# Kernel tuning notes

Hardware: AMD Instinct MI355X
Metric: run time of the kernel (lower is better)

## Reference

```python
import jax, jax.numpy as jnp
import numpy as np

N = 50000       # nodes
E = 1600000     # edges (before self-loops)
IN = 128        # in_channels
HID = 64        # hidden_channels
HEADS = 2
OUT = 16        # out_channels
NEG_SLOPE = 0.2 # PyG GATConv default leaky_relu slope


def setup_inputs() -> dict:
    key = jax.random.key(0)
    ks = jax.random.split(key, 12)
    g = lambda k, shp, s=0.1: (jax.random.normal(k, shp, dtype=jnp.float32) * s)
    return {
        "x": jax.random.normal(ks[0], (N, IN), dtype=jnp.float32),
        "edge_index": jax.random.randint(ks[1], (2, E), 0, N, dtype=jnp.int32),
        # layer 0: in -> hidden, heads concat
        "W0": g(ks[2], (IN, HEADS * HID)),
        "as0": g(ks[3], (HEADS, HID)),
        "ad0": g(ks[4], (HEADS, HID)),
        "b0": jnp.zeros((HEADS * HID,), jnp.float32),
        # layer 1: hidden*heads -> hidden, heads concat
        "W1": g(ks[5], (HEADS * HID, HEADS * HID)),
        "as1": g(ks[6], (HEADS, HID)),
        "ad1": g(ks[7], (HEADS, HID)),
        "b1": jnp.zeros((HEADS * HID,), jnp.float32),
        # layer 2: hidden*heads -> out, heads averaged (concat=False)
        "W2": g(ks[8], (HEADS * HID, HEADS * OUT)),
        "as2": g(ks[9], (HEADS, OUT)),
        "ad2": g(ks[10], (HEADS, OUT)),
        "b2": jnp.zeros((OUT,), jnp.float32),
    }


def gat_conv(x, src, dst, W, a_src, a_dst, b, concat):
    """PyG-style GATConv (inference; self-loops already in src/dst)."""
    n = x.shape[0]
    H, C = a_src.shape
    h = (x @ W).reshape(n, H, C)                      # [N,H,C]
    alpha_s = jnp.einsum('nhc,hc->nh', h, a_src)      # [N,H]
    alpha_d = jnp.einsum('nhc,hc->nh', h, a_dst)      # [N,H]
    e = alpha_s[src] + alpha_d[dst]                   # [E,H]
    e = jax.nn.leaky_relu(e, NEG_SLOPE)
    # softmax over incoming edges per destination node
    m = jax.ops.segment_max(e, dst, num_segments=n)   # [N,H]
    w = jnp.exp(e - m[dst])                           # [E,H]
    denom = jax.ops.segment_sum(w, dst, num_segments=n)
    alpha = w / (denom[dst] + 1e-16)                  # [E,H]
    out = jax.ops.segment_sum(alpha[:, :, None] * h[src], dst, num_segments=n)  # [N,H,C]
    out = out.reshape(n, H * C) if concat else out.mean(axis=1)
    return out + b


def reference(x, edge_index, W0, as0, ad0, b0, W1, as1, ad1, b1, W2, as2, ad2, b2):
    loop = jnp.arange(N, dtype=edge_index.dtype)
    src = jnp.concatenate([edge_index[0], loop])
    dst = jnp.concatenate([edge_index[1], loop])
    h = jax.nn.elu(gat_conv(x, src, dst, W0, as0, ad0, b0, concat=True))
    h = jax.nn.elu(gat_conv(h, src, dst, W1, as1, ad1, b1, concat=True))
    return gat_conv(h, src, dst, W2, as2, ad2, b2, concat=False)
```

## Files before the change

kernel.cpp:

```cpp
#include <hip/hip_runtime.h>
#include <hip/hip_fp16.h>
#include <cstdint>
#include <cstddef>
#include <type_traits>

constexpr int kN   = 50000;
constexpr int kE   = 1600000;
constexpr int kET  = kE + kN;
constexpr float kNEG = 0.2f;
constexpr int NBUCK = (kN + 127) / 128;
constexpr int CAPB  = 5120;
constexpr int PCHUNK = 2048;
constexpr int PGRID = (kET + PCHUNK - 1) / PCHUNK;

typedef _Float16 f16x8 __attribute__((ext_vector_type(8)));
typedef float    f32x4 __attribute__((ext_vector_type(4)));

__global__ __launch_bounds__(256) void partition_kernel(const int* __restrict__ ei,
                                                        int* __restrict__ bcnt,
                                                        unsigned* __restrict__ part) {
  __shared__ int hist[NBUCK];
  __shared__ int resv[NBUCK];
  __shared__ int lcnt[NBUCK];
  const int t = threadIdx.x;
  for (int i = t; i < NBUCK; i += 256) hist[i] = 0;
  __syncthreads();
  const int c0 = blockIdx.x * PCHUNK;
  const int cend = (c0 + PCHUNK < kET) ? c0 + PCHUNK : kET;
  for (int i = c0 + t; i < cend; i += 256) {
    const int dst = (i < kE) ? ei[kE + i] : (i - kE);
    atomicAdd(&hist[dst >> 7], 1);
  }
  __syncthreads();
  for (int i = t; i < NBUCK; i += 256) {
    lcnt[i] = 0;
    if (hist[i]) resv[i] = i * CAPB + atomicAdd(&bcnt[i], hist[i]);
  }
  __syncthreads();
  for (int i = c0 + t; i < cend; i += 256) {
    int src, dst;
    if (i < kE) { src = ei[i]; dst = ei[kE + i]; }
    else        { src = i - kE; dst = src; }
    const int b = dst >> 7;
    const int off = atomicAdd(&lcnt[b], 1);
    part[resv[b] + off] = ((unsigned)(dst & 127) << 16) | (unsigned)src;
  }
}

__global__ __launch_bounds__(512) void finalize_kernel(const unsigned* __restrict__ part,
                                                       const int* __restrict__ bcnt,
                                                       int* __restrict__ row_beg,
                                                       int* __restrict__ row_cnt,
                                                       int* __restrict__ col_src) {
  __shared__ int cnt[128];
  __shared__ int sc[128];
  __shared__ int nbase[128];
  const int b = blockIdx.x, t = threadIdx.x;
  const int lo = b * CAPB;
  const int hi = lo + bcnt[b];
  if (t < 128) cnt[t] = 0;
  __syncthreads();
  for (int j = lo + t; j < hi; j += 512) atomicAdd(&cnt[part[j] >> 16], 1);
  __syncthreads();
  if (t < 128) sc[t] = cnt[t];
  __syncthreads();
  for (int off = 1; off < 128; off <<= 1) {
    int v = 0;
    if (t < 128 && t >= off) v = sc[t - off];
    __syncthreads();
    if (t < 128) sc[t] += v;
    __syncthreads();
  }
  if (t < 128) {
    const int c = cnt[t];
    nbase[t] = lo + sc[t] - c;
    const int node = b * 128 + t;
    if (node < kN) { row_beg[node] = nbase[t]; row_cnt[node] = c; }
    cnt[t] = 0;
  }
  __syncthreads();
  for (int j = lo + t; j < hi; j += 512) {
    const unsigned v = part[j];
    const int nl = v >> 16;
    const int pos = nbase[nl] + atomicAdd(&cnt[nl], 1);
    col_src[pos] = (int)(v & 0xffffu);
  }
}

__global__ __launch_bounds__(256) void prep_w_kernel(
    const float* __restrict__ W0, const float* __restrict__ W1,
    const float* __restrict__ W2, __half* __restrict__ Wt0,
    __half* __restrict__ Wt1, __half* __restrict__ Wt2) {
  int i = blockIdx.x * 256 + threadIdx.x;
  const int stride = gridDim.x * 256;
  for (; i < 16384 * 2 + 4096; i += stride) {
    if (i < 16384) {
      const int k = i >> 7, c = i & 127;
      Wt0[c * 128 + k] = __float2half_rn(W0[i]);
    } else if (i < 32768) {
      const int j = i - 16384, k = j >> 7, c = j & 127;
      Wt1[c * 128 + k] = __float2half_rn(W1[j]);
    } else {
      const int j = i - 32768, k = j >> 5, c = j & 31;
      Wt2[c * 128 + k] = __float2half_rn(W2[j]);
    }
  }
}

template<int NCOL, typename TIN>
__global__ __launch_bounds__(256) void mfma_transform_kernel(
    const TIN* __restrict__ X, const __half* __restrict__ Wt,
    const float* __restrict__ asf, const float* __restrict__ adf,
    __half* __restrict__ H2, float2* __restrict__ AS, float2* __restrict__ AD, int n) {
  constexpr int NT = NCOL / 16;
  const int wid  = threadIdx.x >> 6;
  const int lane = threadIdx.x & 63;
  const int rbase = blockIdx.x * 64 + wid * 16;
  if (rbase >= n) return;
  const int r  = rbase + (lane & 15);
  const int kg = (lane >> 4) * 8;
  const _Float16* __restrict__ Wf = (const _Float16*)Wt;

  f32x4 acc[NT];
#pragma unroll
  for (int t = 0; t < NT; t++) acc[t] = (f32x4){0.f, 0.f, 0.f, 0.f};

#pragma unroll
  for (int kc = 0; kc < 4; kc++) {
    const int kh = kc * 32 + kg;
    f16x8 bfrag;
    if constexpr (std::is_same<TIN, float>::value) {
      const float4 v0 = *(const float4*)(X + (size_t)r * 128 + kh);
      const float4 v1 = *(const float4*)(X + (size_t)r * 128 + kh + 4);
      bfrag[0] = (_Float16)v0.x; bfrag[1] = (_Float16)v0.y;
      bfrag[2] = (_Float16)v0.z; bfrag[3] = (_Float16)v0.w;
      bfrag[4] = (_Float16)v1.x; bfrag[5] = (_Float16)v1.y;
      bfrag[6] = (_Float16)v1.z; bfrag[7] = (_Float16)v1.w;
    } else {
      bfrag = *(const f16x8*)((const _Float16*)X + (size_t)r * 128 + kh);
    }
#pragma unroll
    for (int t = 0; t < NT; t++) {
      const f16x8 afrag = *(const f16x8*)(Wf + (size_t)(t * 16 + (lane & 15)) * 128 + kh);
      acc[t] = __builtin_amdgcn_mfma_f32_16x16x32_f16(afrag, bfrag, acc[t], 0, 0, 0);
    }
  }

  const int c4 = (lane >> 4) * 4;
  float s0 = 0.f, s1 = 0.f, d0 = 0.f, d1 = 0.f;
#pragma unroll
  for (int t = 0; t < NT; t++) {
    const int c0 = t * 16 + c4;
    const float4 av = *(const float4*)(asf + c0);
    const float4 dv = *(const float4*)(adf + c0);
    const float ps = acc[t][0] * av.x + acc[t][1] * av.y + acc[t][2] * av.z + acc[t][3] * av.w;
    const float pd = acc[t][0] * dv.x + acc[t][1] * dv.y + acc[t][2] * dv.z + acc[t][3] * dv.w;
    if (t < NT / 2) { s0 += ps; d0 += pd; } else { s1 += ps; d1 += pd; }
    union { __half2 h[2]; uint2 u; } pk;
    pk.h[0] = __floats2half2_rn(acc[t][0], acc[t][1]);
    pk.h[1] = __floats2half2_rn(acc[t][2], acc[t][3]);
    *(uint2*)(H2 + (size_t)r * NCOL + c0) = pk.u;
  }
#pragma unroll
  for (int off = 16; off <= 32; off <<= 1) {
    s0 += __shfl_xor(s0, off); s1 += __shfl_xor(s1, off);
    d0 += __shfl_xor(d0, off); d1 += __shfl_xor(d1, off);
  }
  if (lane < 16) {
    AS[rbase + lane] = make_float2(s0, s1);
    AD[rbase + lane] = make_float2(d0, d1);
  }
}

template<int C, int MODE, typename TOUT>
__global__ __launch_bounds__(256) void agg_kernel(
    const __half* __restrict__ H2, const float2* __restrict__ AS,
    const float2* __restrict__ AD, const int* __restrict__ row_beg,
    const int* __restrict__ row_cnt, const int* __restrict__ col_src,
    const float* __restrict__ bias, TOUT* __restrict__ OUT) {
  const int wid  = threadIdx.x >> 6;
  const int lane = threadIdx.x & 63;
  const int node = blockIdx.x * 4 + wid;

  const int begin = row_beg[node];
  const int d = row_cnt[node];
  const float2 adn = AD[node];

  int srcv = 0;
  unsigned pkw = 0;
  float sum0 = 0.f, sum1 = 0.f;
  if (lane < d) {
    srcv = col_src[begin + lane];
    const float2 a = AS[srcv];
    float e0 = a.x + adn.x; e0 = (e0 > 0.f) ? e0 : kNEG * e0;
    float e1 = a.y + adn.y; e1 = (e1 > 0.f) ? e1 : kNEG * e1;
    sum0 = __expf(e0); sum1 = __expf(e1);
    const __half2 ph = __floats2half2_rn(sum0, sum1);
    pkw = *(const unsigned*)&ph;
  }
  for (int j = 64 + lane; j < d; j += 64) {
    const int s = col_src[begin + j];
    const float2 a = AS[s];
    float e0 = a.x + adn.x; e0 = (e0 > 0.f) ? e0 : kNEG * e0;
    float e1 = a.y + adn.y; e1 = (e1 > 0.f) ? e1 : kNEG * e1;
    sum0 += __expf(e0); sum1 += __expf(e1);
  }
#pragma unroll
  for (int off = 32; off >= 1; off >>= 1) {
    sum0 += __shfl_xor(sum0, off);
    sum1 += __shfl_xor(sum1, off);
  }
  const float inv0 = 1.0f / (sum0 + 1e-16f);
  const float inv1 = 1.0f / (sum1 + 1e-16f);

  const int dr = (d < 64) ? d : 64;

  if constexpr (MODE == 0) {
    const int e = lane >> 4;
    const int q = lane & 15;
    const int hsel = (q >= 8);
    const unsigned sel = hsel ? 0x03020302u : 0x01000100u;
    const float inv = hsel ? inv1 : inv0;
    float4 a0 = make_float4(0.f, 0.f, 0.f, 0.f);
    float4 a1 = make_float4(0.f, 0.f, 0.f, 0.f);
    for (int j = 0; j < dr; j += 16) {
      const int j0 = j + e, j1 = j + 4 + e, j2 = j + 8 + e, j3 = j + 12 + e;
      const int s0 = __shfl(srcv, j0), s1 = __shfl(srcv, j1),
                s2 = __shfl(srcv, j2), s3 = __shfl(srcv, j3);
      const unsigned p0 = __shfl((int)pkw, j0), p1 = __shfl((int)pkw, j1),
                     p2 = __shfl((int)pkw, j2), p3 = __shfl((int)pkw, j3);
      union { uint4 u; __half2 h[4]; } r0, r1, r2, r3;
      r0.u = *(const uint4*)(H2 + (size_t)s0 * 128 + 8 * q);
      r1.u = *(const uint4*)(H2 + (size_t)s1 * 128 + 8 * q);
      r2.u = *(const uint4*)(H2 + (size_t)s2 * 128 + 8 * q);
      r3.u = *(const uint4*)(H2 + (size_t)s3 * 128 + 8 * q);
      union { unsigned u; __half2 h; } w0, w1, w2, w3;
      w0.u = __builtin_amdgcn_perm(p0, p0, sel);
      w1.u = __builtin_amdgcn_perm(p1, p1, sel);
      w2.u = __builtin_amdgcn_perm(p2, p2, sel);
      w3.u = __builtin_amdgcn_perm(p3, p3, sel);
      __half2 hz; *(unsigned*)&hz = 0u;
      __half2 hc0 = hz, hc1 = hz, hc2 = hz, hc3 = hz;
      hc0 = __hfma2(w0.h, r0.h[0], hc0); hc1 = __hfma2(w0.h, r0.h[1], hc1);
      hc2 = __hfma2(w0.h, r0.h[2], hc2); hc3 = __hfma2(w0.h, r0.h[3], hc3);
      hc0 = __hfma2(w1.h, r1.h[0], hc0); hc1 = __hfma2(w1.h, r1.h[1], hc1);
      hc2 = __hfma2(w1.h, r1.h[2], hc2); hc3 = __hfma2(w1.h, r1.h[3], hc3);
      hc0 = __hfma2(w2.h, r2.h[0], hc0); hc1 = __hfma2(w2.h, r2.h[1], hc1);
      hc2 = __hfma2(w2.h, r2.h[2], hc2); hc3 = __hfma2(w2.h, r2.h[3], hc3);
      hc0 = __hfma2(w3.h, r3.h[0], hc0); hc1 = __hfma2(w3.h, r3.h[1], hc1);
      hc2 = __hfma2(w3.h, r3.h[2], hc2); hc3 = __hfma2(w3.h, r3.h[3], hc3);
      float2 f;
      f = __half22float2(hc0); a0.x += f.x; a0.y += f.y;
      f = __half22float2(hc1); a0.z += f.x; a0.w += f.y;
      f = __half22float2(hc2); a1.x += f.x; a1.y += f.y;
      f = __half22float2(hc3); a1.z += f.x; a1.w += f.y;
    }
    for (int jt = 64 + e; jt < d; jt += 4) {
      const int s = col_src[begin + jt];
      const float2 a = AS[s];
      float e0 = a.x + adn.x; e0 = (e0 > 0.f) ? e0 : kNEG * e0;
      float e1 = a.y + adn.y; e1 = (e1 > 0.f) ? e1 : kNEG * e1;
      const float w = hsel ? __expf(e1) : __expf(e0);
      union { uint4 u; __half2 h[4]; } raw;
      raw.u = *(const uint4*)(H2 + (size_t)s * 128 + 8 * q);
      const float2 f0 = __half22float2(raw.h[0]);
      const float2 f1 = __half22float2(raw.h[1]);
      const float2 f2 = __half22float2(raw.h[2]);
      const float2 f3 = __half22float2(raw.h[3]);
      a0.x = fmaf(w, f0.x, a0.x); a0.y = fmaf(w, f0.y, a0.y);
      a0.z = fmaf(w, f1.x, a0.z); a0.w = fmaf(w, f1.y, a0.w);
      a1.x = fmaf(w, f2.x, a1.x); a1.y = fmaf(w, f2.y, a1.y);
      a1.z = fmaf(w, f3.x, a1.z); a1.w = fmaf(w, f3.y, a1.w);
    }
#pragma unroll
    for (int off = 32; off >= 16; off >>= 1) {
      a0.x += __shfl_xor(a0.x, off); a0.y += __shfl_xor(a0.y, off);
      a0.z += __shfl_xor(a0.z, off); a0.w += __shfl_xor(a0.w, off);
      a1.x += __shfl_xor(a1.x, off); a1.y += __shfl_xor(a1.y, off);
      a1.z += __shfl_xor(a1.z, off); a1.w += __shfl_xor(a1.w, off);
    }
    if (lane < 16) {
      const int ch = 8 * q;
      const float4 b0v = *(const float4*)(bias + ch);
      const float4 b1v = *(const float4*)(bias + ch + 4);
      float4 o0, o1;
      o0.x = a0.x * inv + b0v.x; o0.y = a0.y * inv + b0v.y;
      o0.z = a0.z * inv + b0v.z; o0.w = a0.w * inv + b0v.w;
      o1.x = a1.x * inv + b1v.x; o1.y = a1.y * inv + b1v.y;
      o1.z = a1.z * inv + b1v.z; o1.w = a1.w * inv + b1v.w;
      o0.x = (o0.x > 0.f) ? o0.x : expm1f(o0.x);
      o0.y = (o0.y > 0.f) ? o0.y : expm1f(o0.y);
      o0.z = (o0.z > 0.f) ? o0.z : expm1f(o0.z);
      o0.w = (o0.w > 0.f) ? o0.w : expm1f(o0.w);
      o1.x = (o1.x > 0.f) ? o1.x : expm1f(o1.x);
      o1.y = (o1.y > 0.f) ? o1.y : expm1f(o1.y);
      o1.z = (o1.z > 0.f) ? o1.z : expm1f(o1.z);
      o1.w = (o1.w > 0.f) ? o1.w : expm1f(o1.w);
      union { __half2 h[4]; uint4 u; } pk;
      pk.h[0] = __floats2half2_rn(o0.x, o0.y);
      pk.h[1] = __floats2half2_rn(o0.z, o0.w);
      pk.h[2] = __floats2half2_rn(o1.x, o1.y);
      pk.h[3] = __floats2half2_rn(o1.z, o1.w);
      *(uint4*)((__half*)OUT + (size_t)node * 128 + ch) = pk.u;
    }
  } else {
    const int e = lane >> 3;
    const int q = lane & 7;
    const int hsel = (q >= 4);
    const unsigned sel = hsel ? 0x03020302u : 0x01000100u;
    const float inv = hsel ? inv1 : inv0;
    __half2 hz; *(unsigned*)&hz = 0u;
    __half2 hc0 = hz, hc1 = hz;
    for (int j = 0; j < dr; j += 16) {
      const int j0 = j + e, j1 = j + 8 + e;
      const int s0 = __shfl(srcv, j0), s1 = __shfl(srcv, j1);
      const unsigned p0 = __shfl((int)pkw, j0), p1 = __shfl((int)pkw, j1);
      union { unsigned u; __half2 h; } w0, w1;
      w0.u = __builtin_amdgcn_perm(p0, p0, sel);
      w1.u = __builtin_amdgcn_perm(p1, p1, sel);
      union { uint2 u; __half2 h[2]; } r0, r1;
      r0.u = *(const uint2*)(H2 + (size_t)s0 * 32 + 4 * q);
      r1.u = *(const uint2*)(H2 + (size_t)s1 * 32 + 4 * q);
      hc0 = __hfma2(w0.h, r0.h[0], hc0); hc1 = __hfma2(w0.h, r0.h[1], hc1);
      hc0 = __hfma2(w1.h, r1.h[0], hc0); hc1 = __hfma2(w1.h, r1.h[1], hc1);
    }
    float4 acc;
    float2 f;
    f = __half22float2(hc0); acc.x = f.x; acc.y = f.y;
    f = __half22float2(hc1); acc.z = f.x; acc.w = f.y;
    for (int jt = 64 + e; jt < d; jt += 8) {
      const int s = col_src[begin + jt];
      const float2 a = AS[s];
      float e0 = a.x + adn.x; e0 = (e0 > 0.f) ? e0 : kNEG * e0;
      float e1 = a.y + adn.y; e1 = (e1 > 0.f) ? e1 : kNEG * e1;
      const float w = hsel ? __expf(e1) : __expf(e0);
      union { uint2 u; __half2 h[2]; } raw;
      raw.u = *(const uint2*)(H2 + (size_t)s * 32 + 4 * q);
      const float2 f0 = __half22float2(raw.h[0]);
      const float2 f1 = __half22float2(raw.h[1]);
      acc.x = fmaf(w, f0.x, acc.x); acc.y = fmaf(w, f0.y, acc.y);
      acc.z = fmaf(w, f1.x, acc.z); acc.w = fmaf(w, f1.y, acc.w);
    }
#pragma unroll
    for (int off = 32; off >= 8; off >>= 1) {
      acc.x += __shfl_xor(acc.x, off); acc.y += __shfl_xor(acc.y, off);
      acc.z += __shfl_xor(acc.z, off); acc.w += __shfl_xor(acc.w, off);
    }
    acc.x *= inv; acc.y *= inv; acc.z *= inv; acc.w *= inv;
    const float px = __shfl_xor(acc.x, 4);
    const float py = __shfl_xor(acc.y, 4);
    const float pz = __shfl_xor(acc.z, 4);
    const float pw2 = __shfl_xor(acc.w, 4);
    if (lane < 4) {
      const int ch = 4 * q;
      const float4 bv = *(const float4*)(bias + ch);
      float4 o;
      o.x = 0.5f * (acc.x + px) + bv.x;
      o.y = 0.5f * (acc.y + py) + bv.y;
      o.z = 0.5f * (acc.z + pz) + bv.z;
      o.w = 0.5f * (acc.w + pw2) + bv.w;
      *(float4*)((float*)OUT + (size_t)node * 16 + ch) = o;
    }
  }
}

extern "C" void kernel_launch(void* const* d_in, const int* in_sizes, int n_in,
                              void* d_out, int out_size, void* d_ws, size_t ws_size,
                              hipStream_t stream) {
  const float* x   = (const float*)d_in[0];
  const int*   ei  = (const int*)d_in[1];
  const float* W0  = (const float*)d_in[2];
  const float* as0 = (const float*)d_in[3];
  const float* ad0 = (const float*)d_in[4];
  const float* b0  = (const float*)d_in[5];
  const float* W1  = (const float*)d_in[6];
  const float* as1 = (const float*)d_in[7];
  const float* ad1 = (const float*)d_in[8];
  const float* b1  = (const float*)d_in[9];
  const float* W2  = (const float*)d_in[10];
  const float* as2 = (const float*)d_in[11];
  const float* ad2 = (const float*)d_in[12];
  const float* b2  = (const float*)d_in[13];
  float* out = (float*)d_out;

  size_t off = 0;
  auto alloc = [&](size_t bytes) -> void* {
    void* p = (char*)d_ws + off;
    off += (bytes + 255) & ~(size_t)255;
    return p;
  };
  int*    row_beg = (int*)alloc(sizeof(int) * kN);
  int*    row_cnt = (int*)alloc(sizeof(int) * kN);
  int*    bcnt    = (int*)alloc(sizeof(int) * NBUCK);
  int*    col_src = (int*)alloc(sizeof(int) * (size_t)NBUCK * CAPB);
  float2* AS      = (float2*)alloc(sizeof(float2) * kN);
  float2* AD      = (float2*)alloc(sizeof(float2) * kN);
  __half* H2      = (__half*)alloc(sizeof(__half) * (size_t)kN * 128);
  __half* actA    = (__half*)alloc(sizeof(__half) * (size_t)kN * 128);
  __half* actB    = (__half*)alloc(sizeof(__half) * (size_t)kN * 128);
  __half* Wt0     = (__half*)alloc(sizeof(__half) * 128 * 128);
  __half* Wt1     = (__half*)alloc(sizeof(__half) * 128 * 128);
  __half* Wt2     = (__half*)alloc(sizeof(__half) * 32 * 128);
  unsigned* part  = (unsigned*)actA;
  (void)ws_size; (void)in_sizes; (void)n_in; (void)out_size;

  hipMemsetAsync(bcnt, 0, sizeof(int) * NBUCK, stream);
  prep_w_kernel<<<144, 256, 0, stream>>>(W0, W1, W2, Wt0, Wt1, Wt2);
  partition_kernel<<<PGRID, 256, 0, stream>>>(ei, bcnt, part);
  finalize_kernel<<<NBUCK, 512, 0, stream>>>(part, bcnt, row_beg, row_cnt, col_src);

  const int tgrid = (kN + 63) / 64;
  const int ngrid = kN / 4;

  mfma_transform_kernel<128, float><<<tgrid, 256, 0, stream>>>(x, Wt0, as0, ad0, H2, AS, AD, kN);
  agg_kernel<64, 0, __half><<<ngrid, 256, 0, stream>>>(H2, AS, AD, row_beg, row_cnt, col_src, b0, actA);

  mfma_transform_kernel<128, __half><<<tgrid, 256, 0, stream>>>(actA, Wt1, as1, ad1, H2, AS, AD, kN);
  agg_kernel<64, 0, __half><<<ngrid, 256, 0, stream>>>(H2, AS, AD, row_beg, row_cnt, col_src, b1, actB);

  mfma_transform_kernel<32, __half><<<tgrid, 256, 0, stream>>>(actB, Wt2, as2, ad2, H2, AS, AD, kN);
  agg_kernel<16, 1, float><<<ngrid, 256, 0, stream>>>(H2, AS, AD, row_beg, row_cnt, col_src, b2, out);
}
```

Before: 252.3 us.

## Split hidden features into column quarters and precompute packed normalized edge weights

For the two 128-wide layers, the transform kernel now writes features as four column-quarter slabs, each N×32 halves. A new weight kernel computes the softmax-normalized attention weights per head and packs each one with its 16-bit source index into a record array. A new aggregation kernel then processes one quarter per block, with block ordering chosen so concurrent blocks gather from a single slab. The aim is better cache locality for the gathers and less exponent work inside the aggregation. In exchange it adds an extra kernel launch, writes and reads two record arrays per layer, accumulates fully in fp16, and relies on node ids fitting in 16 bits.

```diff
diff --git a/kernel.cpp b/kernel.cpp
--- a/kernel.cpp
+++ b/kernel.cpp
@@ -12,6 +12,7 @@
 constexpr int CAPB  = 5120;
 constexpr int PCHUNK = 2048;
 constexpr int PGRID = (kET + PCHUNK - 1) / PCHUNK;
+constexpr int QSTRIDE = kN * 32;
 
 typedef _Float16 f16x8 __attribute__((ext_vector_type(8)));
 typedef float    f32x4 __attribute__((ext_vector_type(4)));
@@ -159,7 +160,13 @@
     union { __half2 h[2]; uint2 u; } pk;
     pk.h[0] = __floats2half2_rn(acc[t][0], acc[t][1]);
     pk.h[1] = __floats2half2_rn(acc[t][2], acc[t][3]);
-    *(uint2*)(H2 + (size_t)r * NCOL + c0) = pk.u;
+    if constexpr (NCOL == 128) {
+      const int qq = c0 >> 5;
+      const int co = c0 & 31;
+      *(uint2*)(H2 + (size_t)qq * QSTRIDE + (size_t)r * 32 + co) = pk.u;
+    } else {
+      *(uint2*)(H2 + (size_t)r * NCOL + c0) = pk.u;
+    }
   }
 #pragma unroll
   for (int off = 16; off <= 32; off <<= 1) {
@@ -172,16 +179,162 @@
   }
 }
 
-template<int C, int MODE, typename TOUT>
-__global__ __launch_bounds__(256) void agg_kernel(
+__global__ __launch_bounds__(256) void weight_kernel(
+    const float2* __restrict__ AS, const float2* __restrict__ AD,
+    const int* __restrict__ row_beg, const int* __restrict__ row_cnt,
+    const int* __restrict__ col_src,
+    unsigned* __restrict__ rec0, unsigned* __restrict__ rec1) {
+  const int wid  = threadIdx.x >> 6;
+  const int lane = threadIdx.x & 63;
+  const int node = blockIdx.x * 4 + wid;
+  const int begin = row_beg[node];
+  const int d = row_cnt[node];
+  const float2 adn = AD[node];
+
+  int srcv = 0;
+  float w0 = 0.f, w1 = 0.f;
+  if (lane < d) {
+    srcv = col_src[begin + lane];
+    const float2 a = AS[srcv];
+    float e0 = a.x + adn.x; e0 = (e0 > 0.f) ? e0 : kNEG * e0;
+    float e1 = a.y + adn.y; e1 = (e1 > 0.f) ? e1 : kNEG * e1;
+    w0 = __expf(e0); w1 = __expf(e1);
+  }
+  float sum0 = w0, sum1 = w1;
+  for (int j = 64 + lane; j < d; j += 64) {
+    const int s = col_src[begin + j];
+    const float2 a = AS[s];
+    float e0 = a.x + adn.x; e0 = (e0 > 0.f) ? e0 : kNEG * e0;
+    float e1 = a.y + adn.y; e1 = (e1 > 0.f) ? e1 : kNEG * e1;
+    sum0 += __expf(e0); sum1 += __expf(e1);
+  }
+#pragma unroll
+  for (int off = 32; off >= 1; off >>= 1) {
+    sum0 += __shfl_xor(sum0, off);
+    sum1 += __shfl_xor(sum1, off);
+  }
+  const float inv0 = 1.0f / (sum0 + 1e-16f);
+  const float inv1 = 1.0f / (sum1 + 1e-16f);
+  if (lane < d) {
+    const unsigned h0 = (unsigned)__half_as_ushort(__float2half_rn(w0 * inv0));
+    const unsigned h1 = (unsigned)__half_as_ushort(__float2half_rn(w1 * inv1));
+    rec0[begin + lane] = (unsigned)srcv | (h0 << 16);
+    rec1[begin + lane] = (unsigned)srcv | (h1 << 16);
+  }
+  for (int j = 64 + lane; j < d; j += 64) {
+    const int s = col_src[begin + j];
+    const float2 a = AS[s];
+    float e0 = a.x + adn.x; e0 = (e0 > 0.f) ? e0 : kNEG * e0;
+    float e1 = a.y + adn.y; e1 = (e1 > 0.f) ? e1 : kNEG * e1;
+    const unsigned h0 = (unsigned)__half_as_ushort(__float2half_rn(__expf(e0) * inv0));
+    const unsigned h1 = (unsigned)__half_as_ushort(__float2half_rn(__expf(e1) * inv1));
+    rec0[begin + j] = (unsigned)s | (h0 << 16);
+    rec1[begin + j] = (unsigned)s | (h1 << 16);
+  }
+}
+
+__global__ __launch_bounds__(256) void agg64q_kernel(
+    const __half* __restrict__ H2q, const unsigned* __restrict__ rec0,
+    const unsigned* __restrict__ rec1, const int* __restrict__ row_beg,
+    const int* __restrict__ row_cnt, const float* __restrict__ bias,
+    __half* __restrict__ OUT) {
+  const int bid = blockIdx.x;
+  const int qtr = (bid & 7) >> 1;
+  const int ng  = ((bid >> 3) << 1) | (bid & 1);
+  const int wid  = threadIdx.x >> 6;
+  const int lane = threadIdx.x & 63;
+  const int node = ng * 4 + wid;
+  const int begin = row_beg[node];
+  const int d = row_cnt[node];
+  const unsigned* __restrict__ rec = (qtr >= 2) ? rec1 : rec0;
+  const __half* __restrict__ Hq = H2q + (size_t)qtr * QSTRIDE;
+  const int strm = lane >> 2;
+  const int cq   = lane & 3;
+
+  const unsigned recreg = (lane < d) ? rec[begin + lane] : 0u;
+
+  __half2 hz; *(unsigned*)&hz = 0u;
+  __half2 hc0 = hz, hc1 = hz, hc2 = hz, hc3 = hz;
+  {
+    const unsigned r0 = (unsigned)__shfl((int)recreg, strm);
+    const unsigned r1 = (unsigned)__shfl((int)recreg, 16 + strm);
+    const unsigned r2 = (unsigned)__shfl((int)recreg, 32 + strm);
+    const unsigned r3 = (unsigned)__shfl((int)recreg, 48 + strm);
+    union { uint4 u; __half2 h[4]; } v0, v1, v2, v3;
+    v0.u = *(const uint4*)(Hq + (size_t)(r0 & 0xffffu) * 32 + (cq << 3));
+    v1.u = *(const uint4*)(Hq + (size_t)(r1 & 0xffffu) * 32 + (cq << 3));
+    v2.u = *(const uint4*)(Hq + (size_t)(r2 & 0xffffu) * 32 + (cq << 3));
+    v3.u = *(const uint4*)(Hq + (size_t)(r3 & 0xffffu) * 32 + (cq << 3));
+    union { unsigned u; __half2 h; } w0, w1, w2, w3;
+    w0.u = __builtin_amdgcn_perm(r0, r0, 0x03020302u);
+    w1.u = __builtin_amdgcn_perm(r1, r1, 0x03020302u);
+    w2.u = __builtin_amdgcn_perm(r2, r2, 0x03020302u);
+    w3.u = __builtin_amdgcn_perm(r3, r3, 0x03020302u);
+    hc0 = __hfma2(w0.h, v0.h[0], hc0); hc1 = __hfma2(w0.h, v0.h[1], hc1);
+    hc2 = __hfma2(w0.h, v0.h[2], hc2); hc3 = __hfma2(w0.h, v0.h[3], hc3);
+    hc0 = __hfma2(w1.h, v1.h[0], hc0); hc1 = __hfma2(w1.h, v1.h[1], hc1);
+    hc2 = __hfma2(w1.h, v1.h[2], hc2); hc3 = __hfma2(w1.h, v1.h[3], hc3);
+    hc0 = __hfma2(w2.h, v2.h[0], hc0); hc1 = __hfma2(w2.h, v2.h[1], hc1);
+    hc2 = __hfma2(w2.h, v2.h[2], hc2); hc3 = __hfma2(w2.h, v2.h[3], hc3);
+    hc0 = __hfma2(w3.h, v3.h[0], hc0); hc1 = __hfma2(w3.h, v3.h[1], hc1);
+    hc2 = __hfma2(w3.h, v3.h[2], hc2); hc3 = __hfma2(w3.h, v3.h[3], hc3);
+  }
+  for (int jt = 64 + strm; jt < d; jt += 16) {
+    const unsigned r = rec[begin + jt];
+    union { unsigned u; __half2 h; } wv;
+    wv.u = __builtin_amdgcn_perm(r, r, 0x03020302u);
+    union { uint4 u; __half2 h[4]; } raw;
+    raw.u = *(const uint4*)(Hq + (size_t)(r & 0xffffu) * 32 + (cq << 3));
+    hc0 = __hfma2(wv.h, raw.h[0], hc0);
+    hc1 = __hfma2(wv.h, raw.h[1], hc1);
+    hc2 = __hfma2(wv.h, raw.h[2], hc2);
+    hc3 = __hfma2(wv.h, raw.h[3], hc3);
+  }
+#pragma unroll
+  for (int off = 4; off <= 32; off <<= 1) {
+    union { __half2 h; int i; } a0, a1, a2, a3;
+    a0.h = hc0; a1.h = hc1; a2.h = hc2; a3.h = hc3;
+    a0.i = __shfl_xor(a0.i, off); a1.i = __shfl_xor(a1.i, off);
+    a2.i = __shfl_xor(a2.i, off); a3.i = __shfl_xor(a3.i, off);
+    hc0 = __hadd2(hc0, a0.h); hc1 = __hadd2(hc1, a1.h);
+    hc2 = __hadd2(hc2, a2.h); hc3 = __hadd2(hc3, a3.h);
+  }
+  if (lane < 4) {
+    const int ch = qtr * 32 + lane * 8;
+    const float4 b0v = *(const float4*)(bias + ch);
+    const float4 b1v = *(const float4*)(bias + ch + 4);
+    const float2 f0 = __half22float2(hc0);
+    const float2 f1 = __half22float2(hc1);
+    const float2 f2 = __half22float2(hc2);
+    const float2 f3 = __half22float2(hc3);
+    float4 o0, o1;
+    o0.x = f0.x + b0v.x; o0.y = f0.y + b0v.y; o0.z = f1.x + b0v.z; o0.w = f1.y + b0v.w;
+    o1.x = f2.x + b1v.x; o1.y = f2.y + b1v.y; o1.z = f3.x + b1v.z; o1.w = f3.y + b1v.w;
+    o0.x = (o0.x > 0.f) ? o0.x : expm1f(o0.x);
+    o0.y = (o0.y > 0.f) ? o0.y : expm1f(o0.y);
+    o0.z = (o0.z > 0.f) ? o0.z : expm1f(o0.z);
+    o0.w = (o0.w > 0.f) ? o0.w : expm1f(o0.w);
+    o1.x = (o1.x > 0.f) ? o1.x : expm1f(o1.x);
+    o1.y = (o1.y > 0.f) ? o1.y : expm1f(o1.y);
+    o1.z = (o1.z > 0.f) ? o1.z : expm1f(o1.z);
+    o1.w = (o1.w > 0.f) ? o1.w : expm1f(o1.w);
+    union { __half2 h[4]; uint4 u; } pk;
+    pk.h[0] = __floats2half2_rn(o0.x, o0.y);
+    pk.h[1] = __floats2half2_rn(o0.z, o0.w);
+    pk.h[2] = __floats2half2_rn(o1.x, o1.y);
+    pk.h[3] = __floats2half2_rn(o1.z, o1.w);
+    *(uint4*)(OUT + (size_t)node * 128 + ch) = pk.u;
+  }
+}
+
+__global__ __launch_bounds__(256) void agg16_kernel(
     const __half* __restrict__ H2, const float2* __restrict__ AS,
     const float2* __restrict__ AD, const int* __restrict__ row_beg,
     const int* __restrict__ row_cnt, const int* __restrict__ col_src,
-    const float* __restrict__ bias, TOUT* __restrict__ OUT) {
+    const float* __restrict__ bias, float* __restrict__ OUT) {
   const int wid  = threadIdx.x >> 6;
   const int lane = threadIdx.x & 63;
   const int node = blockIdx.x * 4 + wid;
-
   const int begin = row_beg[node];
   const int d = row_cnt[node];
   const float2 adn = AD[node];
@@ -214,153 +367,62 @@
   const float inv1 = 1.0f / (sum1 + 1e-16f);
 
   const int dr = (d < 64) ? d : 64;
-
-  if constexpr (MODE == 0) {
-    const int e = lane >> 4;
-    const int q = lane & 15;
-    const int hsel = (q >= 8);
-    const unsigned sel = hsel ? 0x03020302u : 0x01000100u;
-    const float inv = hsel ? inv1 : inv0;
-    float4 a0 = make_float4(0.f, 0.f, 0.f, 0.f);
-    float4 a1 = make_float4(0.f, 0.f, 0.f, 0.f);
-    for (int j = 0; j < dr; j += 16) {
-      const int j0 = j + e, j1 = j + 4 + e, j2 = j + 8 + e, j3 = j + 12 + e;
-      const int s0 = __shfl(srcv, j0), s1 = __shfl(srcv, j1),
-                s2 = __shfl(srcv, j2), s3 = __shfl(srcv, j3);
-      const unsigned p0 = __shfl((int)pkw, j0), p1 = __shfl((int)pkw, j1),
-                     p2 = __shfl((int)pkw, j2), p3 = __shfl((int)pkw, j3);
-      union { uint4 u; __half2 h[4]; } r0, r1, r2, r3;
-      r0.u = *(const uint4*)(H2 + (size_t)s0 * 128 + 8 * q);
-      r1.u = *(const uint4*)(H2 + (size_t)s1 * 128 + 8 * q);
-      r2.u = *(const uint4*)(H2 + (size_t)s2 * 128 + 8 * q);
-      r3.u = *(const uint4*)(H2 + (size_t)s3 * 128 + 8 * q);
-      union { unsigned u; __half2 h; } w0, w1, w2, w3;
-      w0.u = __builtin_amdgcn_perm(p0, p0, sel);
-      w1.u = __builtin_amdgcn_perm(p1, p1, sel);
-      w2.u = __builtin_amdgcn_perm(p2, p2, sel);
-      w3.u = __builtin_amdgcn_perm(p3, p3, sel);
-      __half2 hz; *(unsigned*)&hz = 0u;
-      __half2 hc0 = hz, hc1 = hz, hc2 = hz, hc3 = hz;
-      hc0 = __hfma2(w0.h, r0.h[0], hc0); hc1 = __hfma2(w0.h, r0.h[1], hc1);
-      hc2 = __hfma2(w0.h, r0.h[2], hc2); hc3 = __hfma2(w0.h, r0.h[3], hc3);
-      hc0 = __hfma2(w1.h, r1.h[0], hc0); hc1 = __hfma2(w1.h, r1.h[1], hc1);
-      hc2 = __hfma2(w1.h, r1.h[2], hc2); hc3 = __hfma2(w1.h, r1.h[3], hc3);
-      hc0 = __hfma2(w2.h, r2.h[0], hc0); hc1 = __hfma2(w2.h, r2.h[1], hc1);
-      hc2 = __hfma2(w2.h, r2.h[2], hc2); hc3 = __hfma2(w2.h, r2.h[3], hc3);
-      hc0 = __hfma2(w3.h, r3.h[0], hc0); hc1 = __hfma2(w3.h, r3.h[1], hc1);
-      hc2 = __hfma2(w3.h, r3.h[2], hc2); hc3 = __hfma2(w3.h, r3.h[3], hc3);
-      float2 f;
-      f = __half22float2(hc0); a0.x += f.x; a0.y += f.y;
-      f = __half22float2(hc1); a0.z += f.x; a0.w += f.y;
-      f = __half22float2(hc2); a1.x += f.x; a1.y += f.y;
-      f = __half22float2(hc3); a1.z += f.x; a1.w += f.y;
-    }
-    for (int jt = 64 + e; jt < d; jt += 4) {
-      const int s = col_src[begin + jt];
-      const float2 a = AS[s];
-      float e0 = a.x + adn.x; e0 = (e0 > 0.f) ? e0 : kNEG * e0;
-      float e1 = a.y + adn.y; e1 = (e1 > 0.f) ? e1 : kNEG * e1;
-      const float w = hsel ? __expf(e1) : __expf(e0);
-      union { uint4 u; __half2 h[4]; } raw;
-      raw.u = *(const uint4*)(H2 + (size_t)s * 128 + 8 * q);
-      const float2 f0 = __half22float2(raw.h[0]);
-      const float2 f1 = __half22float2(raw.h[1]);
-      const float2 f2 = __half22float2(raw.h[2]);
-      const float2 f3 = __half22float2(raw.h[3]);
-      a0.x = fmaf(w, f0.x, a0.x); a0.y = fmaf(w, f0.y, a0.y);
-      a0.z = fmaf(w, f1.x, a0.z); a0.w = fmaf(w, f1.y, a0.w);
-      a1.x = fmaf(w, f2.x, a1.x); a1.y = fmaf(w, f2.y, a1.y);
-      a1.z = fmaf(w, f3.x, a1.z); a1.w = fmaf(w, f3.y, a1.w);
-    }
-#pragma unroll
-    for (int off = 32; off >= 16; off >>= 1) {
-      a0.x += __shfl_xor(a0.x, off); a0.y += __shfl_xor(a0.y, off);
-      a0.z += __shfl_xor(a0.z, off); a0.w += __shfl_xor(a0.w, off);
-      a1.x += __shfl_xor(a1.x, off); a1.y += __shfl_xor(a1.y, off);
-      a1.z += __shfl_xor(a1.z, off); a1.w += __shfl_xor(a1.w, off);
-    }
-    if (lane < 16) {
-      const int ch = 8 * q;
-      const float4 b0v = *(const float4*)(bias + ch);
-      const float4 b1v = *(const float4*)(bias + ch + 4);
-      float4 o0, o1;
-      o0.x = a0.x * inv + b0v.x; o0.y = a0.y * inv + b0v.y;
-      o0.z = a0.z * inv + b0v.z; o0.w = a0.w * inv + b0v.w;
-      o1.x = a1.x * inv + b1v.x; o1.y = a1.y * inv + b1v.y;
-      o1.z = a1.z * inv + b1v.z; o1.w = a1.w * inv + b1v.w;
-      o0.x = (o0.x > 0.f) ? o0.x : expm1f(o0.x);
-      o0.y = (o0.y > 0.f) ? o0.y : expm1f(o0.y);
-      o0.z = (o0.z > 0.f) ? o0.z : expm1f(o0.z);
-      o0.w = (o0.w > 0.f) ? o0.w : expm1f(o0.w);
-      o1.x = (o1.x > 0.f) ? o1.x : expm1f(o1.x);
-      o1.y = (o1.y > 0.f) ? o1.y : expm1f(o1.y);
-      o1.z = (o1.z > 0.f) ? o1.z : expm1f(o1.z);
-      o1.w = (o1.w > 0.f) ? o1.w : expm1f(o1.w);
-      union { __half2 h[4]; uint4 u; } pk;
-      pk.h[0] = __floats2half2_rn(o0.x, o0.y);
-      pk.h[1] = __floats2half2_rn(o0.z, o0.w);
-      pk.h[2] = __floats2half2_rn(o1.x, o1.y);
-      pk.h[3] = __floats2half2_rn(o1.z, o1.w);
-      *(uint4*)((__half*)OUT + (size_t)node * 128 + ch) = pk.u;
-    }
-  } else {
-    const int e = lane >> 3;
-    const int q = lane & 7;
-    const int hsel = (q >= 4);
-    const unsigned sel = hsel ? 0x03020302u : 0x01000100u;
-    const float inv = hsel ? inv1 : inv0;
-    __half2 hz; *(unsigned*)&hz = 0u;
-    __half2 hc0 = hz, hc1 = hz;
-    for (int j = 0; j < dr; j += 16) {
-      const int j0 = j + e, j1 = j + 8 + e;
-      const int s0 = __shfl(srcv, j0), s1 = __shfl(srcv, j1);
-      const unsigned p0 = __shfl((int)pkw, j0), p1 = __shfl((int)pkw, j1);
-      union { unsigned u; __half2 h; } w0, w1;
-      w0.u = __builtin_amdgcn_perm(p0, p0, sel);
-      w1.u = __builtin_amdgcn_perm(p1, p1, sel);
-      union { uint2 u; __half2 h[2]; } r0, r1;
-      r0.u = *(const uint2*)(H2 + (size_t)s0 * 32 + 4 * q);
-      r1.u = *(const uint2*)(H2 + (size_t)s1 * 32 + 4 * q);
-      hc0 = __hfma2(w0.h, r0.h[0], hc0); hc1 = __hfma2(w0.h, r0.h[1], hc1);
-      hc0 = __hfma2(w1.h, r1.h[0], hc0); hc1 = __hfma2(w1.h, r1.h[1], hc1);
-    }
-    float4 acc;
-    float2 f;
-    f = __half22float2(hc0); acc.x = f.x; acc.y = f.y;
-    f = __half22float2(hc1); acc.z = f.x; acc.w = f.y;
-    for (int jt = 64 + e; jt < d; jt += 8) {
-      const int s = col_src[begin + jt];
-      const float2 a = AS[s];
-      float e0 = a.x + adn.x; e0 = (e0 > 0.f) ? e0 : kNEG * e0;
-      float e1 = a.y + adn.y; e1 = (e1 > 0.f) ? e1 : kNEG * e1;
-      const float w = hsel ? __expf(e1) : __expf(e0);
-      union { uint2 u; __half2 h[2]; } raw;
-      raw.u = *(const uint2*)(H2 + (size_t)s * 32 + 4 * q);
-      const float2 f0 = __half22float2(raw.h[0]);
-      const float2 f1 = __half22float2(raw.h[1]);
-      acc.x = fmaf(w, f0.x, acc.x); acc.y = fmaf(w, f0.y, acc.y);
-      acc.z = fmaf(w, f1.x, acc.z); acc.w = fmaf(w, f1.y, acc.w);
-    }
-#pragma unroll
-    for (int off = 32; off >= 8; off >>= 1) {
-      acc.x += __shfl_xor(acc.x, off); acc.y += __shfl_xor(acc.y, off);
-      acc.z += __shfl_xor(acc.z, off); acc.w += __shfl_xor(acc.w, off);
-    }
-    acc.x *= inv; acc.y *= inv; acc.z *= inv; acc.w *= inv;
-    const float px = __shfl_xor(acc.x, 4);
-    const float py = __shfl_xor(acc.y, 4);
-    const float pz = __shfl_xor(acc.z, 4);
-    const float pw2 = __shfl_xor(acc.w, 4);
-    if (lane < 4) {
-      const int ch = 4 * q;
-      const float4 bv = *(const float4*)(bias + ch);
-      float4 o;
-      o.x = 0.5f * (acc.x + px) + bv.x;
-      o.y = 0.5f * (acc.y + py) + bv.y;
-      o.z = 0.5f * (acc.z + pz) + bv.z;
-      o.w = 0.5f * (acc.w + pw2) + bv.w;
-      *(float4*)((float*)OUT + (size_t)node * 16 + ch) = o;
-    }
+  const int e = lane >> 3;
+  const int q = lane & 7;
+  const int hsel = (q >= 4);
+  const unsigned sel = hsel ? 0x03020302u : 0x01000100u;
+  const float inv = hsel ? inv1 : inv0;
+  __half2 hz; *(unsigned*)&hz = 0u;
+  __half2 hc0 = hz, hc1 = hz;
+  for (int j = 0; j < dr; j += 16) {
+    const int j0 = j + e, j1 = j + 8 + e;
+    const int s0 = __shfl(srcv, j0), s1 = __shfl(srcv, j1);
+    const unsigned p0 = __shfl((int)pkw, j0), p1 = __shfl((int)pkw, j1);
+    union { unsigned u; __half2 h; } w0, w1;
+    w0.u = __builtin_amdgcn_perm(p0, p0, sel);
+    w1.u = __builtin_amdgcn_perm(p1, p1, sel);
+    union { uint2 u; __half2 h[2]; } r0, r1;
+    r0.u = *(const uint2*)(H2 + (size_t)s0 * 32 + 4 * q);
+    r1.u = *(const uint2*)(H2 + (size_t)s1 * 32 + 4 * q);
+    hc0 = __hfma2(w0.h, r0.h[0], hc0); hc1 = __hfma2(w0.h, r0.h[1], hc1);
+    hc0 = __hfma2(w1.h, r1.h[0], hc0); hc1 = __hfma2(w1.h, r1.h[1], hc1);
+  }
+  float4 acc;
+  float2 f;
+  f = __half22float2(hc0); acc.x = f.x; acc.y = f.y;
+  f = __half22float2(hc1); acc.z = f.x; acc.w = f.y;
+  for (int jt = 64 + e; jt < d; jt += 8) {
+    const int s = col_src[begin + jt];
+    const float2 a = AS[s];
+    float e0 = a.x + adn.x; e0 = (e0 > 0.f) ? e0 : kNEG * e0;
+    float e1 = a.y + adn.y; e1 = (e1 > 0.f) ? e1 : kNEG * e1;
+    const float w = hsel ? __expf(e1) : __expf(e0);
+    union { uint2 u; __half2 h[2]; } raw;
+    raw.u = *(const uint2*)(H2 + (size_t)s * 32 + 4 * q);
+    const float2 f0 = __half22float2(raw.h[0]);
+    const float2 f1 = __half22float2(raw.h[1]);
+    acc.x = fmaf(w, f0.x, acc.x); acc.y = fmaf(w, f0.y, acc.y);
+    acc.z = fmaf(w, f1.x, acc.z); acc.w = fmaf(w, f1.y, acc.w);
+  }
+#pragma unroll
+  for (int off = 32; off >= 8; off >>= 1) {
+    acc.x += __shfl_xor(acc.x, off); acc.y += __shfl_xor(acc.y, off);
+    acc.z += __shfl_xor(acc.z, off); acc.w += __shfl_xor(acc.w, off);
+  }
+  acc.x *= inv; acc.y *= inv; acc.z *= inv; acc.w *= inv;
+  const float px = __shfl_xor(acc.x, 4);
+  const float py = __shfl_xor(acc.y, 4);
+  const float pz = __shfl_xor(acc.z, 4);
+  const float pw2 = __shfl_xor(acc.w, 4);
+  if (lane < 4) {
+    const int ch = 4 * q;
+    const float4 bv = *(const float4*)(bias + ch);
+    float4 o;
+    o.x = 0.5f * (acc.x + px) + bv.x;
+    o.y = 0.5f * (acc.y + py) + bv.y;
+    o.z = 0.5f * (acc.z + pz) + bv.z;
+    o.w = 0.5f * (acc.w + pw2) + bv.w;
+    *(float4*)(OUT + (size_t)node * 16 + ch) = o;
   }
 }
 
@@ -389,19 +451,21 @@
     off += (bytes + 255) & ~(size_t)255;
     return p;
   };
-  int*    row_beg = (int*)alloc(sizeof(int) * kN);
-  int*    row_cnt = (int*)alloc(sizeof(int) * kN);
-  int*    bcnt    = (int*)alloc(sizeof(int) * NBUCK);
-  int*    col_src = (int*)alloc(sizeof(int) * (size_t)NBUCK * CAPB);
-  float2* AS      = (float2*)alloc(sizeof(float2) * kN);
-  float2* AD      = (float2*)alloc(sizeof(float2) * kN);
-  __half* H2      = (__half*)alloc(sizeof(__half) * (size_t)kN * 128);
-  __half* actA    = (__half*)alloc(sizeof(__half) * (size_t)kN * 128);
-  __half* actB    = (__half*)alloc(sizeof(__half) * (size_t)kN * 128);
-  __half* Wt0     = (__half*)alloc(sizeof(__half) * 128 * 128);
-  __half* Wt1     = (__half*)alloc(sizeof(__half) * 128 * 128);
-  __half* Wt2     = (__half*)alloc(sizeof(__half) * 32 * 128);
-  unsigned* part  = (unsigned*)actA;
+  int*      row_beg = (int*)alloc(sizeof(int) * kN);
+  int*      row_cnt = (int*)alloc(sizeof(int) * kN);
+  int*      bcnt    = (int*)alloc(sizeof(int) * NBUCK);
+  int*      col_src = (int*)alloc(sizeof(int) * (size_t)NBUCK * CAPB);
+  unsigned* rec0    = (unsigned*)alloc(sizeof(unsigned) * (size_t)NBUCK * CAPB);
+  unsigned* rec1    = (unsigned*)alloc(sizeof(unsigned) * (size_t)NBUCK * CAPB);
+  float2*   AS      = (float2*)alloc(sizeof(float2) * kN);
+  float2*   AD      = (float2*)alloc(sizeof(float2) * kN);
+  __half*   H2      = (__half*)alloc(sizeof(__half) * (size_t)kN * 128);
+  __half*   actA    = (__half*)alloc(sizeof(__half) * (size_t)kN * 128);
+  __half*   actB    = (__half*)alloc(sizeof(__half) * (size_t)kN * 128);
+  __half*   Wt0     = (__half*)alloc(sizeof(__half) * 128 * 128);
+  __half*   Wt1     = (__half*)alloc(sizeof(__half) * 128 * 128);
+  __half*   Wt2     = (__half*)alloc(sizeof(__half) * 32 * 128);
+  unsigned* part    = (unsigned*)actA;
   (void)ws_size; (void)in_sizes; (void)n_in; (void)out_size;
 
   hipMemsetAsync(bcnt, 0, sizeof(int) * NBUCK, stream);
@@ -413,11 +477,13 @@
   const int ngrid = kN / 4;
 
   mfma_transform_kernel<128, float><<<tgrid, 256, 0, stream>>>(x, Wt0, as0, ad0, H2, AS, AD, kN);
-  agg_kernel<64, 0, __half><<<ngrid, 256, 0, stream>>>(H2, AS, AD, row_beg, row_cnt, col_src, b0, actA);
+  weight_kernel<<<ngrid, 256, 0, stream>>>(AS, AD, row_beg, row_cnt, col_src, rec0, rec1);
+  agg64q_kernel<<<kN, 256, 0, stream>>>(H2, rec0, rec1, row_beg, row_cnt, b0, actA);
 
   mfma_transform_kernel<128, __half><<<tgrid, 256, 0, stream>>>(actA, Wt1, as1, ad1, H2, AS, AD, kN);
-  agg_kernel<64, 0, __half><<<ngrid, 256, 0, stream>>>(H2, AS, AD, row_beg, row_cnt, col_src, b1, actB);
+  weight_kernel<<<ngrid, 256, 0, stream>>>(AS, AD, row_beg, row_cnt, col_src, rec0, rec1);
+  agg64q_kernel<<<kN, 256, 0, stream>>>(H2, rec0, rec1, row_beg, row_cnt, b1, actB);
 
   mfma_transform_kernel<32, __half><<<tgrid, 256, 0, stream>>>(actB, Wt2, as2, ad2, H2, AS, AD, kN);
-  agg_kernel<16, 1, float><<<ngrid, 256, 0, stream>>>(H2, AS, AD, row_beg, row_cnt, col_src, b2, out);
-}
+  agg16_kernel<<<ngrid, 256, 0, stream>>>(H2, AS, AD, row_beg, row_cnt, col_src, b2, out);
+}
```

Result: slower. 331.1 us (+31.3%).
